# Kernel optimization log

Hardware: AMD Instinct MI355X
Metric: run time of the kernel (lower is better)

Reference implementation:

```python
import jax, jax.numpy as jnp
import numpy as np


def make_dictionary(T, Drr, Dtheta):
    # rows i=0..T-1; (-Drr)**i == (-1)**i * Drr**i for integer i
    idx = jnp.arange(T, dtype=Drr.dtype)[:, None]                      # [T,1]
    sign = jnp.where(jnp.arange(T)[:, None] % 2 == 0, 1.0, -1.0).astype(Drr.dtype)
    ri = Drr[None, :] ** idx                                           # [T,N]
    c = jnp.cos(idx * Dtheta[None, :])
    s = jnp.sin(idx * Dtheta[None, :])
    dic = jnp.concatenate(
        [jnp.ones((T, 1), Drr.dtype), ri * c, sign * ri * c, ri * s, sign * ri * s],
        axis=1,
    )                                                                  # [T, 1+4N]
    G = jnp.linalg.norm(dic, axis=0)
    G = jnp.where(G == 0, jnp.sqrt(jnp.asarray(T, dic.dtype)), G)
    return dic / G


def softshrink(x, lam):
    return jnp.sign(x) * jnp.maximum(jnp.abs(x) - lam, 0.0)


def fista(D, Y, lambd=0.1, max_iter=100, tol=1e-4):
    # D: [T,K], Y: [B,T,F]
    K = D.shape[1]
    DtD = D.T @ D                                                      # [K,K]
    linv = 1.0 / jnp.linalg.norm(DtD)  # torch.norm(DtD, 2) == Frobenius norm
    DtY = jnp.einsum('tk,btf->bkf', D, Y) * linv                       # [B,K,F]
    A = jnp.eye(K, dtype=D.dtype) - DtD * linv
    lam = lambd * linv
    x0 = jnp.zeros_like(DtY)

    def cond(s):
        _, _, _, it, done = s
        return (it < max_iter) & jnp.logical_not(done)

    def body(s):
        x_old, y_old, t, it, done = s
        x_new = softshrink(jnp.einsum('kj,bjf->bkf', A, y_old) + DtY, lam)
        t_new = (1.0 + jnp.sqrt(1.0 + 4.0 * t * t)) / 2.0
        tt = (t - 1.0) / t_new
        y_new = (1.0 + tt) * x_new - tt * x_old
        conv = jnp.linalg.norm((x_new - x_old).ravel()) / K < tol
        return (x_new, y_new, jnp.where(conv, t, t_new), it + 1, conv)

    s0 = (x0, x0, jnp.asarray(1.0, D.dtype), jnp.asarray(0, jnp.int32),
          jnp.asarray(False))
    x, _, _, _, _ = jax.lax.while_loop(cond, body, s0)
    return x


def setup_inputs() -> dict:
    key = jax.random.key(0)
    k1, k2, k3 = jax.random.split(key, 3)
    return {
        'x': jax.random.normal(k1, (2, 36, 20480), jnp.float32),
        'Drr': jax.random.uniform(k2, (40,), dtype=jnp.float32),
        'Dtheta': jax.random.uniform(k3, (40,), dtype=jnp.float32),
        'T': 36,
    }


def reference(x, Drr, Dtheta, T):
    D = make_dictionary(T, Drr, Dtheta)
    return fista(D, x, lambd=0.1, max_iter=100)
```

## Files before the change

### kernel.cpp

```cpp
#include <hip/hip_runtime.h>
#include <math.h>

typedef _Float16 half8 __attribute__((ext_vector_type(8)));
typedef _Float16 half4 __attribute__((ext_vector_type(4)));
typedef float    f32x4 __attribute__((ext_vector_type(4)));

#define T_DIM 36
#define N_AT 40
#define K_REAL 161
#define MT 11
#define KSM 5
#define KS2 2
#define B_DIM 2
#define F_DIM 20480
#define CB 32
#define NG 2
#define NTHREADS 256
#define SETUP_T 512
#define MAXIT 100
#define YK 200
#define YST 72

#define WS_AFRAG_OFF 64
#define AFRAG_BYTES (MT * KSM * 2 * 1024)
#define WS_DFRAG_OFF (WS_AFRAG_OFF + AFRAG_BYTES)
#define DFRAG_BYTES (MT * KS2 * 2 * 1024)
#define WS_A160_OFF (WS_DFRAG_OFF + DFRAG_BYTES)

#define MFMA16(a, b, c) __builtin_amdgcn_mfma_f32_16x16x32_f16((a), (b), (c), 0, 0, 0)

__global__ void setup_kernel(const float* __restrict__ Drr,
                             const float* __restrict__ Dtheta,
                             float* __restrict__ ws) {
    __shared__ float Dl[K_REAL][T_DIM];
    __shared__ float red[SETUP_T];
    __shared__ float s_linv;
    int tid = threadIdx.x;

    if (tid < K_REAL) {
        float col[T_DIM];
        if (tid == 0) {
            for (int i = 0; i < T_DIM; ++i) col[i] = 1.0f;
        } else {
            int q = (tid - 1) / N_AT, n = (tid - 1) % N_AT;
            float r = Drr[n], th = Dtheta[n];
            float ri = 1.0f;
            for (int i = 0; i < T_DIM; ++i) {
                float c = cosf((float)i * th), s = sinf((float)i * th);
                float sign = (i & 1) ? -1.0f : 1.0f;
                float v;
                if (q == 0)      v = ri * c;
                else if (q == 1) v = sign * ri * c;
                else if (q == 2) v = ri * s;
                else             v = sign * ri * s;
                col[i] = v;
                ri *= r;
            }
        }
        float ss = 0.0f;
        for (int i = 0; i < T_DIM; ++i) ss += col[i] * col[i];
        float G = sqrtf(ss);
        float Ginv = (G == 0.0f) ? (1.0f / sqrtf((float)T_DIM)) : (1.0f / G);
        for (int i = 0; i < T_DIM; ++i) Dl[tid][i] = col[i] * Ginv;
    }
    __syncthreads();

    float local = 0.0f;
    for (int p = tid; p < K_REAL * K_REAL; p += SETUP_T) {
        int a = p / K_REAL, b = p % K_REAL;
        float dot = 0.0f;
        for (int i = 0; i < T_DIM; ++i) dot += Dl[a][i] * Dl[b][i];
        local += dot * dot;
    }
    red[tid] = local;
    __syncthreads();
    if (tid == 0) {
        float tot = 0.0f;
        for (int i = 0; i < SETUP_T; ++i) tot += red[i];
        float linv = 1.0f / sqrtf(tot);
        s_linv = linv;
        ws[0] = linv;
        ws[1] = 0.1f * linv;
    }
    __syncthreads();
    float linv = s_linv;

    _Float16* wsA = (_Float16*)((char*)ws + WS_AFRAG_OFF);
    int lane = tid >> 3, e = tid & 7;
    int fm = lane & 15, fq = lane >> 4;
    for (int p = 0; p < MT * KSM; ++p) {
        int Mt = p / KSM, ks = p % KSM;
        int m = Mt * 16 + fm;
        int k = ks * 32 + fq * 8 + e;
        float v = 0.0f;
        if (m < K_REAL) {
            float dot = 0.0f;
            for (int t = 0; t < T_DIM; ++t) dot += Dl[m][t] * Dl[k][t];
            v = ((m == k) ? 1.0f : 0.0f) - linv * dot;
        }
        _Float16 h = (_Float16)v;
        _Float16 l = (_Float16)(v - (float)h);
        int base = (p * 2) * 512 + lane * 8 + e;
        wsA[base]       = h;
        wsA[base + 512] = l;
    }

    _Float16* wsD = (_Float16*)((char*)ws + WS_DFRAG_OFF);
    for (int p = 0; p < MT * KS2; ++p) {
        int Mt = p / KS2, ks2 = p % KS2;
        int kr = Mt * 16 + fm;
        int t  = ks2 * 32 + fq * 8 + e;
        float v = (kr < K_REAL && t < T_DIM) ? linv * Dl[kr][t] : 0.0f;
        _Float16 h = (_Float16)v;
        _Float16 l = (_Float16)(v - (float)h);
        int base = (p * 2) * 512 + lane * 8 + e;
        wsD[base]       = h;
        wsD[base + 512] = l;
    }

    float* wsC = (float*)((char*)ws + WS_A160_OFF);
    if (tid < MT * 16) {
        int m = tid;
        float v = 0.0f;
        if (m < K_REAL) {
            float dot = 0.0f;
            for (int t = 0; t < T_DIM; ++t) dot += Dl[m][t] * Dl[160][t];
            v = ((m == 160) ? 1.0f : 0.0f) - linv * dot;
        }
        wsC[m] = v;
    }
}

__global__ void __launch_bounds__(NTHREADS, 2)
fista_mfma(const float* __restrict__ Y, const float* __restrict__ ws,
           float* __restrict__ out) {
    __shared__ __align__(16) _Float16 ybuf[2][2][CB][YK];

    const float lam = ((const float*)ws)[1];
    const half8* Afp = (const half8*)((const char*)ws + WS_AFRAG_OFF);
    const half8* Dfp = (const half8*)((const char*)ws + WS_DFRAG_OFF);
    const float* A160 = (const float*)((const char*)ws + WS_A160_OFF);

    const int tid  = threadIdx.x;
    const int lane = tid & 63;
    const int mg   = __builtin_amdgcn_readfirstlane(tid >> 6);
    const int mlc  = (mg == 3) ? 2 : 3;
    const int quad = lane >> 4;
    const int cl   = lane & 15;

    const int blk = blockIdx.x;
    const int b   = blk / (F_DIM / CB);
    const int f0  = (blk % (F_DIM / CB)) * CB;

    _Float16* Yst = &ybuf[1][0][0][0];
    const float* Yb = Y + (size_t)b * T_DIM * F_DIM + f0;
    for (int idx = tid; idx < 64 * CB; idx += NTHREADS) {
        int t = idx / CB, c = idx % CB;
        float v = (t < T_DIM) ? Yb[(size_t)t * F_DIM + c] : 0.0f;
        _Float16 h = (_Float16)v;
        _Float16 l = (_Float16)(v - (float)h);
        Yst[c * YST + t]            = h;
        Yst[CB * YST + c * YST + t] = l;
    }
    int4* zb = (int4*)&ybuf[0][0][0][0];
    for (int idx = tid; idx < (2 * CB * YK * 2) / 16; idx += NTHREADS)
        zb[idx] = int4{0, 0, 0, 0};
    __syncthreads();

    f32x4 dty[3][NG];
    #pragma unroll
    for (int ml = 0; ml < 3; ++ml)
        #pragma unroll
        for (int ng = 0; ng < NG; ++ng) dty[ml][ng] = f32x4{0.f, 0.f, 0.f, 0.f};
    #pragma unroll
    for (int ks2 = 0; ks2 < KS2; ++ks2) {
        #pragma unroll
        for (int ng = 0; ng < NG; ++ng) {
            const _Float16* yp = Yst + (ng * 16 + cl) * YST + ks2 * 32 + quad * 8;
            half8 yh = *(const half8*)yp;
            half8 yl = *(const half8*)(yp + CB * YST);
            #pragma unroll
            for (int ml = 0; ml < 3; ++ml) {
                if (ml < mlc) {
                    int Mt = mg * 3 + ml;
                    half8 dh = Dfp[((Mt * KS2 + ks2) * 2 + 0) * 64 + lane];
                    half8 dl = Dfp[((Mt * KS2 + ks2) * 2 + 1) * 64 + lane];
                    dty[ml][ng] = MFMA16(dh, yh, dty[ml][ng]);
                    dty[ml][ng] = MFMA16(dh, yl, dty[ml][ng]);
                    dty[ml][ng] = MFMA16(dl, yh, dty[ml][ng]);
                }
            }
        }
    }
    __syncthreads();

    half8 Af[3][KSM][2];
    float a160[3][4];
    #pragma unroll
    for (int ml = 0; ml < 3; ++ml) {
        if (ml < mlc) {
            #pragma unroll
            for (int ks = 0; ks < KSM; ++ks)
                #pragma unroll
                for (int term = 0; term < 2; ++term)
                    Af[ml][ks][term] =
                        Afp[(((mg * 3 + ml) * KSM + ks) * 2 + term) * 64 + lane];
            #pragma unroll
            for (int r = 0; r < 4; ++r)
                a160[ml][r] = A160[(mg * 3 + ml) * 16 + quad * 4 + r];
        }
    }

    float xold[3][NG][4];
    #pragma unroll
    for (int ml = 0; ml < 3; ++ml)
        #pragma unroll
        for (int ng = 0; ng < NG; ++ng)
            #pragma unroll
            for (int r = 0; r < 4; ++r) xold[ml][ng][r] = 0.0f;

    float tm = 1.0f;
    int p = 0;
    for (int it = 0; it < MAXIT; ++it) {
        f32x4 acc[3][NG];
        #pragma unroll
        for (int ml = 0; ml < 3; ++ml)
            #pragma unroll
            for (int ng = 0; ng < NG; ++ng) acc[ml][ng] = dty[ml][ng];

        #pragma unroll
        for (int ng = 0; ng < NG; ++ng) {
            float y160 = (float)ybuf[p][0][ng * 16 + cl][160]
                       + (float)ybuf[p][1][ng * 16 + cl][160];
            #pragma unroll
            for (int ml = 0; ml < 3; ++ml)
                if (ml < mlc)
                    #pragma unroll
                    for (int r = 0; r < 4; ++r)
                        acc[ml][ng][r] += a160[ml][r] * y160;
        }

        #pragma unroll
        for (int ks = 0; ks < KSM; ++ks) {
            #pragma unroll
            for (int ng = 0; ng < NG; ++ng) {
                const _Float16* yp = &ybuf[p][0][ng * 16 + cl][ks * 32 + quad * 8];
                half8 yh = *(const half8*)yp;
                half8 yl = *(const half8*)(yp + CB * YK);
                #pragma unroll
                for (int ml = 0; ml < 3; ++ml) {
                    if (ml < mlc) {
                        acc[ml][ng] = MFMA16(Af[ml][ks][0], yh, acc[ml][ng]);
                        acc[ml][ng] = MFMA16(Af[ml][ks][0], yl, acc[ml][ng]);
                        acc[ml][ng] = MFMA16(Af[ml][ks][1], yh, acc[ml][ng]);
                    }
                }
            }
        }

        float tn = 0.5f * (1.0f + sqrtf(1.0f + 4.0f * tm * tm));
        float tt = (tm - 1.0f) / tn;
        tm = tn;

        #pragma unroll
        for (int ml = 0; ml < 3; ++ml) {
            if (ml < mlc) {
                #pragma unroll
                for (int ng = 0; ng < NG; ++ng) {
                    half4 hv, lv;
                    #pragma unroll
                    for (int r = 0; r < 4; ++r) {
                        float v  = acc[ml][ng][r];
                        float s  = fmaxf(fabsf(v) - lam, 0.0f);
                        float xn = copysignf(s, v);
                        float yn = (1.0f + tt) * xn - tt * xold[ml][ng][r];
                        xold[ml][ng][r] = xn;
                        _Float16 h = (_Float16)yn;
                        hv[r] = h;
                        lv[r] = (_Float16)(yn - (float)h);
                    }
                    int k0 = (mg * 3 + ml) * 16 + quad * 4;
                    *(half4*)&ybuf[1 - p][0][ng * 16 + cl][k0] = hv;
                    *(half4*)&ybuf[1 - p][1][ng * 16 + cl][k0] = lv;
                }
            }
        }
        __syncthreads();
        p ^= 1;
    }

    #pragma unroll
    for (int ng = 0; ng < NG; ++ng) {
        float* ob = out + (size_t)b * K_REAL * F_DIM + f0 + ng * 16 + cl;
        #pragma unroll
        for (int ml = 0; ml < 3; ++ml)
            if (ml < mlc)
                #pragma unroll
                for (int r = 0; r < 4; ++r) {
                    int k = (mg * 3 + ml) * 16 + quad * 4 + r;
                    if (k < K_REAL) ob[(size_t)k * F_DIM] = xold[ml][ng][r];
                }
    }
}

extern "C" void kernel_launch(void* const* d_in, const int* in_sizes, int n_in,
                              void* d_out, int out_size, void* d_ws, size_t ws_size,
                              hipStream_t stream) {
    const float* x      = (const float*)d_in[0];
    const float* Drr    = (const float*)d_in[1];
    const float* Dtheta = (const float*)d_in[2];
    float* out = (float*)d_out;
    float* ws  = (float*)d_ws;

    hipLaunchKernelGGL(setup_kernel, dim3(1), dim3(SETUP_T), 0, stream,
                       Drr, Dtheta, ws);
    hipLaunchKernelGGL(fista_mfma, dim3((B_DIM * F_DIM) / CB), dim3(NTHREADS),
                       0, stream, x, ws, out);
}
```

Measured before the change: 682.5 us.

## Split FISTA grid into full and half-width blocks to balance the tail wave

The launch now uses 1024 blocks that each own 32 columns plus 512 blocks that each own only 16 columns, instead of 1280 uniform 32-column blocks. The aim is to cut the tail-wave imbalance when the uniform grid does not divide evenly across the CUs at two blocks per CU. Half-width blocks skip the second column group's MFMAs, LDS traffic and stores. They still pay the full per-iteration barrier and latency cost, and every block now evaluates extra runtime branches.

```diff
diff --git a/kernel.cpp b/kernel.cpp
--- a/kernel.cpp
+++ b/kernel.cpp
@@ -14,12 +14,13 @@
 #define B_DIM 2
 #define F_DIM 20480
 #define CB 32
-#define NG 2
 #define NTHREADS 256
 #define SETUP_T 512
 #define MAXIT 100
 #define YK 200
 #define YST 72
+#define NBLK_NG2 1024
+#define NBLK_TOTAL 1536
 
 #define WS_AFRAG_OFF 64
 #define AFRAG_BYTES (MT * KSM * 2 * 1024)
@@ -148,46 +149,56 @@
     const int quad = lane >> 4;
     const int cl   = lane & 15;
 
-    const int blk = blockIdx.x;
-    const int b   = blk / (F_DIM / CB);
-    const int f0  = (blk % (F_DIM / CB)) * CB;
+    const int blk  = blockIdx.x;
+    const bool two = (blk < NBLK_NG2);
+    const int g0   = two ? (blk * 32)
+                         : (NBLK_NG2 * 32 + (blk - NBLK_NG2) * 16);
+    const int b    = g0 / F_DIM;
+    const int f0   = g0 % F_DIM;
+    const int cbb  = two ? 32 : 16;
+    const int pgsel = two ? (mg & 1) : 0;
 
     _Float16* Yst = &ybuf[1][0][0][0];
     const float* Yb = Y + (size_t)b * T_DIM * F_DIM + f0;
-    for (int idx = tid; idx < 64 * CB; idx += NTHREADS) {
-        int t = idx / CB, c = idx % CB;
-        float v = (t < T_DIM) ? Yb[(size_t)t * F_DIM + c] : 0.0f;
-        _Float16 h = (_Float16)v;
-        _Float16 l = (_Float16)(v - (float)h);
-        Yst[c * YST + t]            = h;
-        Yst[CB * YST + c * YST + t] = l;
+    for (int idx = tid; idx < 64 * 32; idx += NTHREADS) {
+        int t = idx / 32, c = idx % 32;
+        if (c < cbb) {
+            float v = (t < T_DIM) ? Yb[(size_t)t * F_DIM + c] : 0.0f;
+            _Float16 h = (_Float16)v;
+            _Float16 l = (_Float16)(v - (float)h);
+            Yst[c * YST + t]            = h;
+            Yst[CB * YST + c * YST + t] = l;
+        }
     }
     int4* zb = (int4*)&ybuf[0][0][0][0];
     for (int idx = tid; idx < (2 * CB * YK * 2) / 16; idx += NTHREADS)
         zb[idx] = int4{0, 0, 0, 0};
     __syncthreads();
 
-    f32x4 dty[3][NG];
+    f32x4 dty[3][2];
     #pragma unroll
     for (int ml = 0; ml < 3; ++ml)
         #pragma unroll
-        for (int ng = 0; ng < NG; ++ng) dty[ml][ng] = f32x4{0.f, 0.f, 0.f, 0.f};
+        for (int ng = 0; ng < 2; ++ng) dty[ml][ng] = f32x4{0.f, 0.f, 0.f, 0.f};
     #pragma unroll
     for (int ks2 = 0; ks2 < KS2; ++ks2) {
         #pragma unroll
-        for (int ng = 0; ng < NG; ++ng) {
-            const _Float16* yp = Yst + (ng * 16 + cl) * YST + ks2 * 32 + quad * 8;
-            half8 yh = *(const half8*)yp;
-            half8 yl = *(const half8*)(yp + CB * YST);
-            #pragma unroll
-            for (int ml = 0; ml < 3; ++ml) {
-                if (ml < mlc) {
-                    int Mt = mg * 3 + ml;
-                    half8 dh = Dfp[((Mt * KS2 + ks2) * 2 + 0) * 64 + lane];
-                    half8 dl = Dfp[((Mt * KS2 + ks2) * 2 + 1) * 64 + lane];
-                    dty[ml][ng] = MFMA16(dh, yh, dty[ml][ng]);
-                    dty[ml][ng] = MFMA16(dh, yl, dty[ml][ng]);
-                    dty[ml][ng] = MFMA16(dl, yh, dty[ml][ng]);
+        for (int ng = 0; ng < 2; ++ng) {
+            if (ng == 0 || two) {
+                int pg = ng ^ pgsel;
+                const _Float16* yp = Yst + (pg * 16 + cl) * YST + ks2 * 32 + quad * 8;
+                half8 yh = *(const half8*)yp;
+                half8 yl = *(const half8*)(yp + CB * YST);
+                #pragma unroll
+                for (int ml = 0; ml < 3; ++ml) {
+                    if (ml < mlc) {
+                        int Mt = mg * 3 + ml;
+                        half8 dh = Dfp[((Mt * KS2 + ks2) * 2 + 0) * 64 + lane];
+                        half8 dl = Dfp[((Mt * KS2 + ks2) * 2 + 1) * 64 + lane];
+                        dty[ml][ng] = MFMA16(dh, yh, dty[ml][ng]);
+                        dty[ml][ng] = MFMA16(dh, yl, dty[ml][ng]);
+                        dty[ml][ng] = MFMA16(dl, yh, dty[ml][ng]);
+                    }
                 }
             }
         }
@@ -211,95 +222,108 @@
         }
     }
 
-    float xold[3][NG][4];
+    float xold[3][2][4];
     #pragma unroll
     for (int ml = 0; ml < 3; ++ml)
         #pragma unroll
-        for (int ng = 0; ng < NG; ++ng)
+        for (int ng = 0; ng < 2; ++ng)
             #pragma unroll
             for (int r = 0; r < 4; ++r) xold[ml][ng][r] = 0.0f;
 
     float tm = 1.0f;
     int p = 0;
     for (int it = 0; it < MAXIT; ++it) {
-        f32x4 acc[3][NG];
+        f32x4 acc[3][2];
         #pragma unroll
         for (int ml = 0; ml < 3; ++ml)
             #pragma unroll
-            for (int ng = 0; ng < NG; ++ng) acc[ml][ng] = dty[ml][ng];
-
-        #pragma unroll
-        for (int ng = 0; ng < NG; ++ng) {
-            float y160 = (float)ybuf[p][0][ng * 16 + cl][160]
-                       + (float)ybuf[p][1][ng * 16 + cl][160];
+            for (int ng = 0; ng < 2; ++ng) acc[ml][ng] = dty[ml][ng];
+
+        #pragma unroll
+        for (int ng = 0; ng < 2; ++ng) {
+            if (ng == 0 || two) {
+                int pg = ng ^ pgsel;
+                float y160 = (float)ybuf[p][0][pg * 16 + cl][160]
+                           + (float)ybuf[p][1][pg * 16 + cl][160];
+                #pragma unroll
+                for (int ml = 0; ml < 3; ++ml)
+                    if (ml < mlc)
+                        #pragma unroll
+                        for (int r = 0; r < 4; ++r)
+                            acc[ml][ng][r] += a160[ml][r] * y160;
+            }
+        }
+
+        #pragma unroll
+        for (int ks = 0; ks < KSM; ++ks) {
+            #pragma unroll
+            for (int ng = 0; ng < 2; ++ng) {
+                if (ng == 0 || two) {
+                    int pg = ng ^ pgsel;
+                    const _Float16* yp =
+                        &ybuf[p][0][pg * 16 + cl][ks * 32 + quad * 8];
+                    half8 yh = *(const half8*)yp;
+                    half8 yl = *(const half8*)(yp + CB * YK);
+                    #pragma unroll
+                    for (int ml = 0; ml < 3; ++ml) {
+                        if (ml < mlc) {
+                            acc[ml][ng] = MFMA16(Af[ml][ks][0], yh, acc[ml][ng]);
+                            acc[ml][ng] = MFMA16(Af[ml][ks][0], yl, acc[ml][ng]);
+                            acc[ml][ng] = MFMA16(Af[ml][ks][1], yh, acc[ml][ng]);
+                        }
+                    }
+                }
+            }
+        }
+
+        float tn = 0.5f * (1.0f + sqrtf(1.0f + 4.0f * tm * tm));
+        float tt = (tm - 1.0f) / tn;
+        tm = tn;
+
+        #pragma unroll
+        for (int ml = 0; ml < 3; ++ml) {
+            if (ml < mlc) {
+                #pragma unroll
+                for (int ng = 0; ng < 2; ++ng) {
+                    if (ng == 0 || two) {
+                        int pg = ng ^ pgsel;
+                        half4 hv, lv;
+                        #pragma unroll
+                        for (int r = 0; r < 4; ++r) {
+                            float v  = acc[ml][ng][r];
+                            float s  = fmaxf(fabsf(v) - lam, 0.0f);
+                            float xn = copysignf(s, v);
+                            float yn = (1.0f + tt) * xn - tt * xold[ml][ng][r];
+                            xold[ml][ng][r] = xn;
+                            _Float16 h = (_Float16)yn;
+                            hv[r] = h;
+                            lv[r] = (_Float16)(yn - (float)h);
+                        }
+                        int k0 = (mg * 3 + ml) * 16 + quad * 4;
+                        *(half4*)&ybuf[1 - p][0][pg * 16 + cl][k0] = hv;
+                        *(half4*)&ybuf[1 - p][1][pg * 16 + cl][k0] = lv;
+                    }
+                }
+            }
+        }
+        __syncthreads();
+        p ^= 1;
+    }
+
+    #pragma unroll
+    for (int ng = 0; ng < 2; ++ng) {
+        if (ng == 0 || two) {
+            int pg = ng ^ pgsel;
+            float* ob = out + (size_t)b * K_REAL * F_DIM + f0 + pg * 16 + cl;
             #pragma unroll
             for (int ml = 0; ml < 3; ++ml)
                 if (ml < mlc)
                     #pragma unroll
-                    for (int r = 0; r < 4; ++r)
-                        acc[ml][ng][r] += a160[ml][r] * y160;
-        }
-
-        #pragma unroll
-        for (int ks = 0; ks < KSM; ++ks) {
-            #pragma unroll
-            for (int ng = 0; ng < NG; ++ng) {
-                const _Float16* yp = &ybuf[p][0][ng * 16 + cl][ks * 32 + quad * 8];
-                half8 yh = *(const half8*)yp;
-                half8 yl = *(const half8*)(yp + CB * YK);
-                #pragma unroll
-                for (int ml = 0; ml < 3; ++ml) {
-                    if (ml < mlc) {
-                        acc[ml][ng] = MFMA16(Af[ml][ks][0], yh, acc[ml][ng]);
-                        acc[ml][ng] = MFMA16(Af[ml][ks][0], yl, acc[ml][ng]);
-                        acc[ml][ng] = MFMA16(Af[ml][ks][1], yh, acc[ml][ng]);
+                    for (int r = 0; r < 4; ++r) {
+                        int k = (mg * 3 + ml) * 16 + quad * 4 + r;
+                        if (k < K_REAL) ob[(size_t)k * F_DIM] = xold[ml][ng][r];
                     }
-                }
-            }
-        }
-
-        float tn = 0.5f * (1.0f + sqrtf(1.0f + 4.0f * tm * tm));
-        float tt = (tm - 1.0f) / tn;
-        tm = tn;
-
-        #pragma unroll
-        for (int ml = 0; ml < 3; ++ml) {
-            if (ml < mlc) {
-                #pragma unroll
-                for (int ng = 0; ng < NG; ++ng) {
-                    half4 hv, lv;
-                    #pragma unroll
-                    for (int r = 0; r < 4; ++r) {
-                        float v  = acc[ml][ng][r];
-                        float s  = fmaxf(fabsf(v) - lam, 0.0f);
-                        float xn = copysignf(s, v);
-                        float yn = (1.0f + tt) * xn - tt * xold[ml][ng][r];
-                        xold[ml][ng][r] = xn;
-                        _Float16 h = (_Float16)yn;
-                        hv[r] = h;
-                        lv[r] = (_Float16)(yn - (float)h);
-                    }
-                    int k0 = (mg * 3 + ml) * 16 + quad * 4;
-                    *(half4*)&ybuf[1 - p][0][ng * 16 + cl][k0] = hv;
-                    *(half4*)&ybuf[1 - p][1][ng * 16 + cl][k0] = lv;
-                }
-            }
-        }
-        __syncthreads();
-        p ^= 1;
-    }
-
-    #pragma unroll
-    for (int ng = 0; ng < NG; ++ng) {
-        float* ob = out + (size_t)b * K_REAL * F_DIM + f0 + ng * 16 + cl;
-        #pragma unroll
-        for (int ml = 0; ml < 3; ++ml)
-            if (ml < mlc)
-                #pragma unroll
-                for (int r = 0; r < 4; ++r) {
-                    int k = (mg * 3 + ml) * 16 + quad * 4 + r;
-                    if (k < K_REAL) ob[(size_t)k * F_DIM] = xold[ml][ng][r];
-                }
+        }
     }
 }
 
@@ -314,6 +338,6 @@
 
     hipLaunchKernelGGL(setup_kernel, dim3(1), dim3(SETUP_T), 0, stream,
                        Drr, Dtheta, ws);
-    hipLaunchKernelGGL(fista_mfma, dim3((B_DIM * F_DIM) / CB), dim3(NTHREADS),
+    hipLaunchKernelGGL(fista_mfma, dim3(NBLK_TOTAL), dim3(NTHREADS),
                        0, stream, x, ws, out);
 }
```

After: 696.5 us. +2.1%, slower.
